# Kernel optimization log

Measured on AMD Instinct MI355X. Metric: run time of the kernel, lower is better.

The kernel has to match this reference:

```python
import math
import jax, jax.numpy as jnp
import numpy as np

B, S, D, H, L = 2, 2048, 1024, 16, 4
HD = D // H  # head_dim = 64


def setup_inputs() -> dict:
    key = jax.random.key(0)
    ks = jax.random.split(key, 7)
    scale = 0.02
    return {
        "x": jax.random.normal(ks[0], (B, S, D), jnp.float32),
        "past_q": jax.random.normal(ks[1], (B, H, S, L, HD), jnp.float32),
        "past_v": jax.random.normal(ks[2], (B, H, S, L, HD), jnp.float32),
        "Wq": jax.random.normal(ks[3], (D, D), jnp.float32) * scale,
        "bq": jnp.zeros((D,), jnp.float32),
        "Wo": jax.random.normal(ks[4], (D, D), jnp.float32) * scale,
        "bo": jnp.zeros((D,), jnp.float32),
    }


def reference(x, past_q, past_v, Wq, bq, Wo, bo):
    b, s, d = x.shape
    # q_proj then split heads -> [B,H,S,hd]
    q = (x @ Wq.T + bq).reshape(b, s, H, HD).transpose(0, 2, 1, 3)
    v = x.reshape(b, s, H, HD).transpose(0, 2, 1, 3)
    inv = 1.0 / math.sqrt(HD)
    # token scores: Q used as both query and key, causal mask
    token_scores = jnp.einsum("bhqd,bhkd->bhqk", q, q) * inv
    causal = jnp.triu(jnp.ones((s, s), bool), k=1)
    token_scores = jnp.where(causal, -jnp.inf, token_scores)
    # memory scores: elementwise mul-sum over L cached layers -> [B,H,S,L]
    mem_scores = jnp.einsum("bhsd,bhsld->bhsl", q, past_q) * inv
    scores = jnp.concatenate([token_scores, mem_scores], axis=-1)  # [B,H,S,S+L]
    weights = jax.nn.softmax(scores, axis=-1)
    tw, mw = weights[..., :s], weights[..., s:]
    token_ctx = jnp.einsum("bhqk,bhkd->bhqd", tw, v)
    mem_ctx = jnp.einsum("bhsl,bhsld->bhsd", mw, past_v)
    ctx = (token_ctx + mem_ctx).transpose(0, 2, 1, 3).reshape(b, s, d)
    return jax.nn.gelu(ctx @ Wo.T + bo, approximate=False)
```

## Files before the change

### kernel.cpp

```cpp
#include <hip/hip_runtime.h>
#include <hip/hip_bf16.h>
#include <math.h>

#define S_LEN 2048
#define DIM   1024
#define NH    16
#define NL    4
#define NB    2
#define PARTS_PER_BH 80
#define ALPHA 0.42466086f

typedef __attribute__((ext_vector_type(8))) short bf16x8;
typedef __attribute__((ext_vector_type(4))) float f32x4;
typedef unsigned short u16;

__device__ __forceinline__ float bf2f(u16 u) {
  union { unsigned int i; float f; } x; x.i = ((unsigned int)u) << 16; return x.f;
}
__device__ __forceinline__ u16 f2bf(float f) {
  union { float f; unsigned int i; } x; x.f = f;
  unsigned int r = x.i + 0x7fffu + ((x.i >> 16) & 1u);
  return (u16)(r >> 16);
}
__device__ __forceinline__ u16 f2bfq(float f) {
  __hip_bfloat16 h = __float2bfloat16(f);
  return *reinterpret_cast<u16*>(&h);
}

__device__ __forceinline__ void g2l16(const void* g, void* l) {
  __builtin_amdgcn_global_load_lds(
      (const __attribute__((address_space(1))) void*)g,
      (__attribute__((address_space(3))) void*)l, 16, 0, 0);
}

__device__ __forceinline__ float gelu_fast(float v) {
  float y = 0.79788456f * (v + 0.044715f * v * v * v);
  float e = exp2f(y * 2.88539008f);
  float t = 1.0f - 2.0f / (e + 1.0f);
  return 0.5f * v * (1.0f + t);
}

__global__ __launch_bounds__(256)
void cvt_all(const float* __restrict__ x, const float* __restrict__ wq,
             const float* __restrict__ wo, u16* __restrict__ ox,
             u16* __restrict__ owq, u16* __restrict__ owo, int n4x, int n4w) {
  int i = blockIdx.x * blockDim.x + threadIdx.x;
  const float* src; u16* dst; int j;
  if (i < n4x)            { src = x;  dst = ox;  j = i; }
  else if (i < n4x + n4w) { src = wq; dst = owq; j = i - n4x; }
  else                    { src = wo; dst = owo; j = i - n4x - n4w;
                            if (j >= n4w) return; }
  float4 v = ((const float4*)src)[j];
  ushort4 o;
  o.x = f2bf(v.x); o.y = f2bf(v.y); o.z = f2bf(v.z); o.w = f2bf(v.w);
  ((ushort4*)dst)[j] = o;
}

template <bool GELU, typename OT>
__global__ __launch_bounds__(256)
void gemm_bt(const u16* __restrict__ A, const u16* __restrict__ Bt,
             const float* __restrict__ bias, OT* __restrict__ C,
             int M, int N, int K, float oscale) {
  __shared__ u16 As[2][128 * 64];
  __shared__ u16 Bs[2][64 * 64];
  const int lane = threadIdx.x & 63, wave = threadIdx.x >> 6;
  const int ln = lane & 15, g = lane >> 4;
  const int nwg = gridDim.x * gridDim.y;
  const int flat = blockIdx.y * gridDim.x + blockIdx.x;
  const int swz = (flat & 7) * (nwg >> 3) + (flat >> 3);
  const int m0 = (swz / gridDim.x) * 128, n0 = (swz % gridDim.x) * 64;
  const int wm = wave >> 1, wn = wave & 1;
  f32x4 acc[4][2] = {};

  auto stage = [&](int buf, int k0) {
#pragma unroll
    for (int rd = 0; rd < 6; ++rd) {
      int ch = rd * 4 + wave;
      if (ch < 16) {
        int flatb = ch * 1024 + lane * 16;
        int row = flatb >> 7;
        int within = (flatb & 127) ^ ((row & 7) << 4);
        g2l16((const char*)A + ((size_t)(m0 + row) * K + k0) * 2 + within,
              (char*)As[buf] + ch * 1024);
      } else {
        int flatb = (ch - 16) * 1024 + lane * 16;
        int row = flatb >> 7;
        int within = (flatb & 127) ^ ((row & 7) << 4);
        g2l16((const char*)Bt + ((size_t)(n0 + row) * K + k0) * 2 + within,
              (char*)Bs[buf] + (ch - 16) * 1024);
      }
    }
  };

  stage(0, 0);
  __syncthreads();
  const int NT = K / 64;
  for (int t = 0; t < NT; ++t) {
    const int cur = t & 1;
    if (t + 1 < NT) stage(cur ^ 1, (t + 1) * 64);
#pragma unroll
    for (int kc = 0; kc < 2; ++kc) {
      bf16x8 af[4], bfr[2];
#pragma unroll
      for (int i = 0; i < 4; ++i) {
        int ra = wm * 64 + i * 16 + ln;
        af[i] = *(const bf16x8*)((const char*)As[cur] + ra * 128 +
                                 ((kc * 64 + g * 16) ^ ((ra & 7) << 4)));
      }
#pragma unroll
      for (int j = 0; j < 2; ++j) {
        int rb = wn * 32 + j * 16 + ln;
        bfr[j] = *(const bf16x8*)((const char*)Bs[cur] + rb * 128 +
                                  ((kc * 64 + g * 16) ^ ((rb & 7) << 4)));
      }
#pragma unroll
      for (int i = 0; i < 4; ++i)
#pragma unroll
        for (int j = 0; j < 2; ++j)
          acc[i][j] = __builtin_amdgcn_mfma_f32_16x16x32_bf16(af[i], bfr[j], acc[i][j], 0, 0, 0);
    }
    __syncthreads();
  }

#pragma unroll
  for (int j = 0; j < 2; ++j) {
    int gc = n0 + wn * 32 + j * 16 + ln;
    float bv = bias[gc];
#pragma unroll
    for (int i = 0; i < 4; ++i) {
      int gr0 = m0 + wm * 64 + i * 16 + g * 4;
#pragma unroll
      for (int r = 0; r < 4; ++r) {
        float v = acc[i][j][r] + bv;
        if constexpr (GELU) v = gelu_fast(v);
        v *= oscale;
        if constexpr (sizeof(OT) == 2) C[(size_t)(gr0 + r) * N + gc] = (OT)f2bf(v);
        else                           C[(size_t)(gr0 + r) * N + gc] = (OT)v;
      }
    }
  }
}

__global__ __launch_bounds__(256)
void attn(const u16* __restrict__ Q, const u16* __restrict__ Xb,
          u16* __restrict__ CTXP, float* __restrict__ MP, float* __restrict__ LP) {
  __shared__ u16 Ks[2][64 * 64];
  __shared__ u16 Vt[2][64 * 64];
  __shared__ u16 Pw[4][16 * 64];

  const int lane = threadIdx.x & 63, wave = threadIdx.x >> 6;
  const int ln = lane & 15, g = lane >> 4;
  const int h = blockIdx.y, b = blockIdx.z;

  const int p = blockIdx.x;
  int qt, chunk;
  if (p < 8)       { qt = p;                          chunk = 0; }
  else if (p < 24) { int i = p - 8;  qt = 8 + (i >> 1);  chunk = i & 1; }
  else if (p < 48) { int i = p - 24; qt = 16 + i / 3;    chunk = i % 3; }
  else             { int i = p - 48; qt = 24 + (i >> 2); chunk = i & 3; }
  const int kt0 = chunk * 8;
  const int kt1e = kt0 + 8 < qt + 1 ? kt0 + 8 : qt + 1;

  const size_t qrow = (size_t)b * S_LEN + qt * 64 + wave * 16 + ln;
  const bf16x8 qa0 = *(const bf16x8*)(Q + qrow * DIM + h * 64 + g * 8);
  const bf16x8 qa1 = *(const bf16x8*)(Q + qrow * DIM + h * 64 + 32 + g * 8);

  f32x4 acc[4] = {};
  float m_run = -INFINITY;
  float l_run = 0.f;

  const int tid = threadIdx.x;
  const int vr0 = (tid >> 3) * 2;
  const int vc0 = (tid & 7) * 8;
#define VSWZ(c) ((((c) ^ ((c) >> 3)) & 7) << 4)

  {
    const u16* xsrc = Xb + ((size_t)b * S_LEN + kt0 * 64 + vr0) * DIM + h * 64 + vc0;
    bf16x8 r0 = *(const bf16x8*)xsrc;
    bf16x8 r1 = *(const bf16x8*)(xsrc + DIM);
#pragma unroll
    for (int rd = 0; rd < 2; ++rd) {
      int ch = rd * 4 + wave;
      int flat = ch * 1024 + lane * 16;
      int row = flat >> 7;
      int within = (flat & 127) ^ ((row & 7) << 4);
      g2l16((const char*)Q + (((size_t)b * S_LEN + kt0 * 64 + row) * DIM + h * 64) * 2 + within,
            (char*)Ks[0] + ch * 1024);
    }
#pragma unroll
    for (int j = 0; j < 8; ++j) {
      int c = vc0 + j;
      unsigned int pack = (unsigned int)(u16)r0[j] | ((unsigned int)(u16)r1[j] << 16);
      *(unsigned int*)((char*)Vt[0] + c * 128 + ((vr0 * 2) ^ VSWZ(c))) = pack;
    }
  }
  __syncthreads();

  for (int kt = kt0; kt < kt1e; ++kt) {
    const int cur = (kt - kt0) & 1, nxt = cur ^ 1;
    const bool more = (kt + 1 < kt1e);
    bf16x8 nr0, nr1;
    if (more) {
      const u16* xsrc = Xb + ((size_t)b * S_LEN + (kt + 1) * 64 + vr0) * DIM + h * 64 + vc0;
      nr0 = *(const bf16x8*)xsrc;
      nr1 = *(const bf16x8*)(xsrc + DIM);
#pragma unroll
      for (int rd = 0; rd < 2; ++rd) {
        int ch = rd * 4 + wave;
        int flat = ch * 1024 + lane * 16;
        int row = flat >> 7;
        int within = (flat & 127) ^ ((row & 7) << 4);
        g2l16((const char*)Q + (((size_t)b * S_LEN + (kt + 1) * 64 + row) * DIM + h * 64) * 2 + within,
              (char*)Ks[nxt] + ch * 1024);
      }
      __builtin_amdgcn_sched_barrier(0);
    }

    float pv_[4][4];
#pragma unroll
    for (int sub = 0; sub < 4; ++sub) {
      int kr = sub * 16 + ln;
      bf16x8 kb0 = *(const bf16x8*)((const char*)Ks[cur] + kr * 128 + ((g * 16) ^ ((kr & 7) << 4)));
      bf16x8 kb1 = *(const bf16x8*)((const char*)Ks[cur] + kr * 128 + ((64 + g * 16) ^ ((kr & 7) << 4)));
      f32x4 c = {};
      c = __builtin_amdgcn_mfma_f32_16x16x32_bf16(kb0, qa0, c, 0, 0, 0);
      c = __builtin_amdgcn_mfma_f32_16x16x32_bf16(kb1, qa1, c, 0, 0, 0);
      if (kt == qt) {
#pragma unroll
        for (int r = 0; r < 4; ++r) {
          int key = sub * 16 + g * 4 + r;
          int qi = wave * 16 + ln;
          pv_[sub][r] = (key > qi) ? -INFINITY : c[r];
        }
      } else {
#pragma unroll
        for (int r = 0; r < 4; ++r) pv_[sub][r] = c[r];
      }
    }

    float pmax = pv_[0][0];
#pragma unroll
    for (int sub = 0; sub < 4; ++sub)
#pragma unroll
      for (int r = 0; r < 4; ++r) pmax = fmaxf(pmax, pv_[sub][r]);
    pmax = fmaxf(pmax, __shfl_xor(pmax, 16));
    pmax = fmaxf(pmax, __shfl_xor(pmax, 32));

    if (!__all(pmax <= m_run + 8.0f)) {
      float m_new = fmaxf(m_run, pmax);
      float scl = exp2f(m_run - m_new);
      m_run = m_new;
      l_run *= scl;
#pragma unroll
      for (int r = 0; r < 4; ++r) {
        float s = __shfl(scl, g * 4 + r);
#pragma unroll
        for (int ns = 0; ns < 4; ++ns) acc[ns][r] *= s;
      }
    }

    float lsum = 0.f;
#pragma unroll
    for (int sub = 0; sub < 4; ++sub)
#pragma unroll
      for (int r = 0; r < 4; ++r) {
        pv_[sub][r] = exp2f(pv_[sub][r] - m_run);
        lsum += pv_[sub][r];
      }
    lsum += __shfl_xor(lsum, 16);
    lsum += __shfl_xor(lsum, 32);
    l_run += lsum;

#pragma unroll
    for (int sub = 0; sub < 4; ++sub) {
      uint2 val;
      val.x = (unsigned int)f2bfq(pv_[sub][0]) | ((unsigned int)f2bfq(pv_[sub][1]) << 16);
      val.y = (unsigned int)f2bfq(pv_[sub][2]) | ((unsigned int)f2bfq(pv_[sub][3]) << 16);
      *(uint2*)((char*)Pw[wave] + ln * 128 + ((sub * 32 + g * 8) ^ ((ln & 7) << 4))) = val;
    }

    bf16x8 pa0 = *(const bf16x8*)((const char*)Pw[wave] + ln * 128 + ((g * 16) ^ ((ln & 7) << 4)));
    bf16x8 pa1 = *(const bf16x8*)((const char*)Pw[wave] + ln * 128 + ((64 + g * 16) ^ ((ln & 7) << 4)));
#pragma unroll
    for (int ns = 0; ns < 4; ++ns) {
      int vr = ns * 16 + ln;
      bf16x8 vb0 = *(const bf16x8*)((const char*)Vt[cur] + vr * 128 + ((g * 16) ^ VSWZ(vr)));
      bf16x8 vb1 = *(const bf16x8*)((const char*)Vt[cur] + vr * 128 + ((64 + g * 16) ^ VSWZ(vr)));
      acc[ns] = __builtin_amdgcn_mfma_f32_16x16x32_bf16(pa0, vb0, acc[ns], 0, 0, 0);
      acc[ns] = __builtin_amdgcn_mfma_f32_16x16x32_bf16(pa1, vb1, acc[ns], 0, 0, 0);
    }

    if (more) {
#pragma unroll
      for (int j = 0; j < 8; ++j) {
        int c = vc0 + j;
        unsigned int pack = (unsigned int)(u16)nr0[j] | ((unsigned int)(u16)nr1[j] << 16);
        *(unsigned int*)((char*)Vt[nxt] + c * 128 + ((vr0 * 2) ^ VSWZ(c))) = pack;
      }
    }
    __syncthreads();
  }

  const size_t slot = ((size_t)(b * NH + h)) * PARTS_PER_BH + p;
#pragma unroll
  for (int ns = 0; ns < 4; ++ns)
#pragma unroll
    for (int r = 0; r < 4; ++r) {
      int qr = wave * 16 + g * 4 + r;
      CTXP[slot * 4096 + (size_t)qr * 64 + ns * 16 + ln] = f2bfq(acc[ns][r]);
    }
  if (lane < 16) {
    MP[slot * 64 + wave * 16 + lane] = m_run;
    LP[slot * 64 + wave * 16 + lane] = l_run;
  }
}

__global__ __launch_bounds__(256)
void finalize(const u16* __restrict__ Q, const float* __restrict__ PQ,
              const float* __restrict__ PV, const u16* __restrict__ CTXP,
              const float* __restrict__ MP, const float* __restrict__ LP,
              u16* __restrict__ Cout) {
  const int lane = threadIdx.x & 63, wave = threadIdx.x >> 6;
  const size_t row = (size_t)blockIdx.x * 4 + wave;
  const int s = (int)(row & (S_LEN - 1));
  const int h = (int)((row >> 11) & (NH - 1));
  const int b = (int)(row >> 15);

  const int qt = s >> 6, G = qt >> 3, parts = G + 1;
  const int baseG[4] = {0, 8, 24, 48};
  const int p0 = baseG[G] + (qt & 7) * parts;
  const size_t slot0 = ((size_t)(b * NH + h)) * PARTS_PER_BH + p0;
  const int sr = s & 63;

  float mc[4], lc[4];
  float m_tok = -INFINITY;
#pragma unroll
  for (int c = 0; c < 4; ++c)
    if (c < parts) {
      mc[c] = MP[(slot0 + c) * 64 + sr];
      lc[c] = LP[(slot0 + c) * 64 + sr];
      m_tok = fmaxf(m_tok, mc[c]);
    }
  float l_tok = 0.f, cd = 0.f;
#pragma unroll
  for (int c = 0; c < 4; ++c)
    if (c < parts) {
      float w = exp2f(mc[c] - m_tok);
      l_tok += w * lc[c];
      cd += w * bf2f(CTXP[(slot0 + c) * 4096 + (size_t)sr * 64 + lane]);
    }

  const float qd = bf2f(Q[((size_t)b * S_LEN + s) * DIM + h * 64 + lane]);
  const float* pq = PQ + row * (NL * 64);
  const float* pv = PV + row * (NL * 64);
  float msc[NL];
  float m_fin = m_tok;
#pragma unroll
  for (int lm = 0; lm < NL; ++lm) {
    float prod = qd * pq[lm * 64 + lane];
#pragma unroll
    for (int o = 1; o < 64; o <<= 1) prod += __shfl_xor(prod, o);
    msc[lm] = prod * ALPHA;
    m_fin = fmaxf(m_fin, msc[lm]);
  }
  const float a = exp2f(m_tok - m_fin);
  float l_fin = l_tok * a;
  cd *= a;
#pragma unroll
  for (int lm = 0; lm < NL; ++lm) {
    float w = exp2f(msc[lm] - m_fin);
    l_fin += w;
    cd += w * pv[lm * 64 + lane];
  }
  Cout[((size_t)b * S_LEN + s) * DIM + h * 64 + lane] = f2bf(cd / l_fin);
}

extern "C" void kernel_launch(void* const* d_in, const int* in_sizes, int n_in,
                              void* d_out, int out_size, void* d_ws, size_t ws_size,
                              hipStream_t stream) {
  const float* x  = (const float*)d_in[0];
  const float* pq = (const float*)d_in[1];
  const float* pv = (const float*)d_in[2];
  const float* Wq = (const float*)d_in[3];
  const float* bq = (const float*)d_in[4];
  const float* Wo = (const float*)d_in[5];
  const float* bo = (const float*)d_in[6];
  float* out = (float*)d_out;

  const int M = NB * S_LEN;
  u16*   Qws  = (u16*)d_ws;
  u16*   Cws  = Qws + (size_t)M * DIM;
  u16*   xbf  = Cws + (size_t)M * DIM;
  u16*   Wqbf = xbf + (size_t)M * DIM;
  u16*   Wobf = Wqbf + (size_t)DIM * DIM;
  u16*   CTXP = Wobf + (size_t)DIM * DIM;
  float* MP   = (float*)(CTXP + (size_t)NB * NH * PARTS_PER_BH * 4096);
  float* LP   = MP + (size_t)NB * NH * PARTS_PER_BH * 64;

  const int n4x = M * DIM / 4, n4w = DIM * DIM / 4;
  cvt_all<<<(n4x + 2 * n4w + 255) / 256, 256, 0, stream>>>(
      x, Wq, Wo, xbf, Wqbf, Wobf, n4x, n4w);

  gemm_bt<false, u16><<<dim3(DIM / 64, M / 128), 256, 0, stream>>>(
      xbf, Wqbf, bq, Qws, M, DIM, DIM, ALPHA);
  attn<<<dim3(PARTS_PER_BH, NH, NB), 256, 0, stream>>>(Qws, xbf, CTXP, MP, LP);
  finalize<<<NB * NH * S_LEN / 4, 256, 0, stream>>>(Qws, pq, pv, CTXP, MP, LP, Cws);
  gemm_bt<true, float><<<dim3(DIM / 64, M / 128), 256, 0, stream>>>(
      Cws, Wobf, bo, out, M, DIM, DIM, 1.0f);
}
```

Before: 140.7 us.

## Precompute LDS addresses, unroll attention loop by two, add setprio and occupancy hint

```diff
diff --git a/kernel.cpp b/kernel.cpp
--- a/kernel.cpp
+++ b/kernel.cpp
@@ -13,6 +13,8 @@
 typedef __attribute__((ext_vector_type(8))) short bf16x8;
 typedef __attribute__((ext_vector_type(4))) float f32x4;
 typedef unsigned short u16;
+
+template <int N> struct Tag { static constexpr int cur = N; };
 
 __device__ __forceinline__ float bf2f(u16 u) {
   union { unsigned int i; float f; } x; x.i = ((unsigned int)u) << 16; return x.f;
@@ -65,10 +67,7 @@
   __shared__ u16 Bs[2][64 * 64];
   const int lane = threadIdx.x & 63, wave = threadIdx.x >> 6;
   const int ln = lane & 15, g = lane >> 4;
-  const int nwg = gridDim.x * gridDim.y;
-  const int flat = blockIdx.y * gridDim.x + blockIdx.x;
-  const int swz = (flat & 7) * (nwg >> 3) + (flat >> 3);
-  const int m0 = (swz / gridDim.x) * 128, n0 = (swz % gridDim.x) * 64;
+  const int m0 = blockIdx.y * 128, n0 = blockIdx.x * 64;
   const int wm = wave >> 1, wn = wave & 1;
   f32x4 acc[4][2] = {};
 
@@ -141,12 +140,10 @@
   }
 }
 
-__global__ __launch_bounds__(256)
+__global__ __launch_bounds__(256, 4)
 void attn(const u16* __restrict__ Q, const u16* __restrict__ Xb,
           u16* __restrict__ CTXP, float* __restrict__ MP, float* __restrict__ LP) {
-  __shared__ u16 Ks[2][64 * 64];
-  __shared__ u16 Vt[2][64 * 64];
-  __shared__ u16 Pw[4][16 * 64];
+  __shared__ __attribute__((aligned(16))) char lds[40960];
 
   const int lane = threadIdx.x & 63, wave = threadIdx.x >> 6;
   const int ln = lane & 15, g = lane >> 4;
@@ -165,63 +162,85 @@
   const bf16x8 qa0 = *(const bf16x8*)(Q + qrow * DIM + h * 64 + g * 8);
   const bf16x8 qa1 = *(const bf16x8*)(Q + qrow * DIM + h * 64 + 32 + g * 8);
 
+  const int tid = threadIdx.x;
+  const int vr0 = (tid >> 3) * 2;
+  const int vc0 = (tid & 7) * 8;
+  const int t7 = tid & 7;
+  const int sw7 = (ln & 7) << 4;
+  const int kbase0 = ln * 128 + ((g * 16) ^ sw7);
+  const int kbase1 = ln * 128 + ((64 + g * 16) ^ sw7);
+  const int swb = (ln & 7) ^ (ln >> 3);
+  int vrd0[4], vrd1[4];
+#pragma unroll
+  for (int ns = 0; ns < 4; ++ns) {
+    int sw = (swb ^ (ns * 2)) << 4;
+    vrd0[ns] = ln * 128 + ((g * 16) ^ sw);
+    vrd1[ns] = ln * 128 + ((64 + g * 16) ^ sw);
+  }
+  int vwr[8];
+#pragma unroll
+  for (int j = 0; j < 8; ++j)
+    vwr[j] = (vc0 + j) * 128 + ((vr0 * 2) ^ ((j ^ t7) << 4));
+  int pst[4];
+#pragma unroll
+  for (int sub = 0; sub < 4; ++sub)
+    pst[sub] = 32768 + wave * 2048 + ln * 128 + ((sub * 32 + g * 8) ^ sw7);
+  const int prd0 = 32768 + wave * 2048 + ln * 128 + ((g * 16) ^ sw7);
+  const int prd1 = 32768 + wave * 2048 + ln * 128 + ((64 + g * 16) ^ sw7);
+  int ksrc[2];
+#pragma unroll
+  for (int rd = 0; rd < 2; ++rd) {
+    int ch = rd * 4 + wave;
+    int flat = ch * 1024 + lane * 16;
+    int row = flat >> 7;
+    ksrc[rd] = row * (DIM * 2) + ((flat & 127) ^ ((row & 7) << 4));
+  }
+
+  const size_t STEP = (size_t)64 * DIM * 2;
+  const char* kq = (const char*)(Q + ((size_t)b * S_LEN + (size_t)kt0 * 64) * DIM + h * 64);
+  const char* xv = (const char*)(Xb + ((size_t)b * S_LEN + (size_t)kt0 * 64 + vr0) * DIM + h * 64 + vc0);
+
   f32x4 acc[4] = {};
   float m_run = -INFINITY;
   float l_run = 0.f;
 
-  const int tid = threadIdx.x;
-  const int vr0 = (tid >> 3) * 2;
-  const int vc0 = (tid & 7) * 8;
-#define VSWZ(c) ((((c) ^ ((c) >> 3)) & 7) << 4)
-
   {
-    const u16* xsrc = Xb + ((size_t)b * S_LEN + kt0 * 64 + vr0) * DIM + h * 64 + vc0;
-    bf16x8 r0 = *(const bf16x8*)xsrc;
-    bf16x8 r1 = *(const bf16x8*)(xsrc + DIM);
-#pragma unroll
-    for (int rd = 0; rd < 2; ++rd) {
-      int ch = rd * 4 + wave;
-      int flat = ch * 1024 + lane * 16;
-      int row = flat >> 7;
-      int within = (flat & 127) ^ ((row & 7) << 4);
-      g2l16((const char*)Q + (((size_t)b * S_LEN + kt0 * 64 + row) * DIM + h * 64) * 2 + within,
-            (char*)Ks[0] + ch * 1024);
-    }
+    bf16x8 r0 = *(const bf16x8*)xv;
+    bf16x8 r1 = *(const bf16x8*)(xv + DIM * 2);
+#pragma unroll
+    for (int rd = 0; rd < 2; ++rd)
+      g2l16(kq + ksrc[rd], lds + (rd * 4 + wave) * 1024);
 #pragma unroll
     for (int j = 0; j < 8; ++j) {
-      int c = vc0 + j;
       unsigned int pack = (unsigned int)(u16)r0[j] | ((unsigned int)(u16)r1[j] << 16);
-      *(unsigned int*)((char*)Vt[0] + c * 128 + ((vr0 * 2) ^ VSWZ(c))) = pack;
+      *(unsigned int*)(lds + 16384 + vwr[j]) = pack;
     }
   }
   __syncthreads();
 
-  for (int kt = kt0; kt < kt1e; ++kt) {
-    const int cur = (kt - kt0) & 1, nxt = cur ^ 1;
+  int kt = kt0;
+  auto body = [&](auto tag) {
+    constexpr int CUR = decltype(tag)::cur;
+    constexpr int NXT = CUR ^ 1;
     const bool more = (kt + 1 < kt1e);
     bf16x8 nr0, nr1;
     if (more) {
-      const u16* xsrc = Xb + ((size_t)b * S_LEN + (kt + 1) * 64 + vr0) * DIM + h * 64 + vc0;
-      nr0 = *(const bf16x8*)xsrc;
-      nr1 = *(const bf16x8*)(xsrc + DIM);
-#pragma unroll
-      for (int rd = 0; rd < 2; ++rd) {
-        int ch = rd * 4 + wave;
-        int flat = ch * 1024 + lane * 16;
-        int row = flat >> 7;
-        int within = (flat & 127) ^ ((row & 7) << 4);
-        g2l16((const char*)Q + (((size_t)b * S_LEN + (kt + 1) * 64 + row) * DIM + h * 64) * 2 + within,
-              (char*)Ks[nxt] + ch * 1024);
-      }
+      const char* nxv = xv + STEP;
+      nr0 = *(const bf16x8*)nxv;
+      nr1 = *(const bf16x8*)(nxv + DIM * 2);
+      const char* nkq = kq + STEP;
+#pragma unroll
+      for (int rd = 0; rd < 2; ++rd)
+        g2l16(nkq + ksrc[rd], lds + NXT * 8192 + (rd * 4 + wave) * 1024);
       __builtin_amdgcn_sched_barrier(0);
     }
 
     float pv_[4][4];
+    __builtin_amdgcn_s_setprio(1);
 #pragma unroll
     for (int sub = 0; sub < 4; ++sub) {
-      int kr = sub * 16 + ln;
-      bf16x8 kb0 = *(const bf16x8*)((const char*)Ks[cur] + kr * 128 + ((g * 16) ^ ((kr & 7) << 4)));
-      bf16x8 kb1 = *(const bf16x8*)((const char*)Ks[cur] + kr * 128 + ((64 + g * 16) ^ ((kr & 7) << 4)));
+      bf16x8 kb0 = *(const bf16x8*)(lds + CUR * 8192 + sub * 2048 + kbase0);
+      bf16x8 kb1 = *(const bf16x8*)(lds + CUR * 8192 + sub * 2048 + kbase1);
       f32x4 c = {};
       c = __builtin_amdgcn_mfma_f32_16x16x32_bf16(kb0, qa0, c, 0, 0, 0);
       c = __builtin_amdgcn_mfma_f32_16x16x32_bf16(kb1, qa1, c, 0, 0, 0);
@@ -229,14 +248,14 @@
 #pragma unroll
         for (int r = 0; r < 4; ++r) {
           int key = sub * 16 + g * 4 + r;
-          int qi = wave * 16 + ln;
-          pv_[sub][r] = (key > qi) ? -INFINITY : c[r];
+          pv_[sub][r] = (key > wave * 16 + ln) ? -INFINITY : c[r];
         }
       } else {
 #pragma unroll
         for (int r = 0; r < 4; ++r) pv_[sub][r] = c[r];
       }
     }
+    __builtin_amdgcn_s_setprio(0);
 
     float pmax = pv_[0][0];
 #pragma unroll
@@ -276,29 +295,37 @@
       uint2 val;
       val.x = (unsigned int)f2bfq(pv_[sub][0]) | ((unsigned int)f2bfq(pv_[sub][1]) << 16);
       val.y = (unsigned int)f2bfq(pv_[sub][2]) | ((unsigned int)f2bfq(pv_[sub][3]) << 16);
-      *(uint2*)((char*)Pw[wave] + ln * 128 + ((sub * 32 + g * 8) ^ ((ln & 7) << 4))) = val;
-    }
-
-    bf16x8 pa0 = *(const bf16x8*)((const char*)Pw[wave] + ln * 128 + ((g * 16) ^ ((ln & 7) << 4)));
-    bf16x8 pa1 = *(const bf16x8*)((const char*)Pw[wave] + ln * 128 + ((64 + g * 16) ^ ((ln & 7) << 4)));
+      *(uint2*)(lds + pst[sub]) = val;
+    }
+
+    bf16x8 pa0 = *(const bf16x8*)(lds + prd0);
+    bf16x8 pa1 = *(const bf16x8*)(lds + prd1);
+    __builtin_amdgcn_s_setprio(1);
 #pragma unroll
     for (int ns = 0; ns < 4; ++ns) {
-      int vr = ns * 16 + ln;
-      bf16x8 vb0 = *(const bf16x8*)((const char*)Vt[cur] + vr * 128 + ((g * 16) ^ VSWZ(vr)));
-      bf16x8 vb1 = *(const bf16x8*)((const char*)Vt[cur] + vr * 128 + ((64 + g * 16) ^ VSWZ(vr)));
+      bf16x8 vb0 = *(const bf16x8*)(lds + 16384 + CUR * 8192 + ns * 2048 + vrd0[ns]);
+      bf16x8 vb1 = *(const bf16x8*)(lds + 16384 + CUR * 8192 + ns * 2048 + vrd1[ns]);
       acc[ns] = __builtin_amdgcn_mfma_f32_16x16x32_bf16(pa0, vb0, acc[ns], 0, 0, 0);
       acc[ns] = __builtin_amdgcn_mfma_f32_16x16x32_bf16(pa1, vb1, acc[ns], 0, 0, 0);
     }
+    __builtin_amdgcn_s_setprio(0);
 
     if (more) {
 #pragma unroll
       for (int j = 0; j < 8; ++j) {
-        int c = vc0 + j;
         unsigned int pack = (unsigned int)(u16)nr0[j] | ((unsigned int)(u16)nr1[j] << 16);
-        *(unsigned int*)((char*)Vt[nxt] + c * 128 + ((vr0 * 2) ^ VSWZ(c))) = pack;
+        *(unsigned int*)(lds + 16384 + NXT * 8192 + vwr[j]) = pack;
       }
     }
     __syncthreads();
+    kq += STEP; xv += STEP;
+  };
+
+  for (;;) {
+    body(Tag<0>{});
+    if (++kt >= kt1e) break;
+    body(Tag<1>{});
+    if (++kt >= kt1e) break;
   }
 
   const size_t slot = ((size_t)(b * NH + h)) * PARTS_PER_BH + p;
```

Measured after the change: 129.7 us. 7.8% less time.
